# Optimization experiments

Measured on AMD Instinct MI355X. Metric: run time of the kernel, lower is better.

Reference implementation:

```python
import jax, jax.numpy as jnp
import numpy as np

NEG_SLOPE = 0.2

def _gat_conv(x, src, dst, W, a_src, a_dst, b, heads, out_ch, concat):
    N = x.shape[0]
    h = (x @ W).reshape(N, heads, out_ch)                      # [N,H,C]
    al_s = jnp.einsum('nhc,hc->nh', h, a_src)                  # [N,H]
    al_d = jnp.einsum('nhc,hc->nh', h, a_dst)
    e = jax.nn.leaky_relu(al_s[src] + al_d[dst], NEG_SLOPE)    # [E,H]
    emax = jax.ops.segment_max(e, dst, num_segments=N)         # [N,H]
    ex = jnp.exp(e - emax[dst])
    denom = jax.ops.segment_sum(ex, dst, num_segments=N)
    alpha = ex / denom[dst]                                    # [E,H]
    msg = h[src] * alpha[:, :, None]                           # [E,H,C]
    out = jax.ops.segment_sum(msg, dst, num_segments=N)        # [N,H,C]
    if concat:
        out = out.reshape(N, heads * out_ch)
    else:
        out = out.mean(axis=1)
    return out + b

def _add_self_loops(edge_index, N):
    loops = jnp.arange(N, dtype=edge_index.dtype)
    src = jnp.concatenate([edge_index[0], loops])
    dst = jnp.concatenate([edge_index[1], loops])
    return src, dst

def setup_inputs() -> dict:
    key = jax.random.key(0)
    ks = jax.random.split(key, 16)
    N, E, Fin, C, H, G, OUT = 50000, 1600000, 128, 32, 8, 256, 64
    s = 0.05
    inp = {
        'x': jax.random.normal(ks[0], (N, Fin), jnp.float32),
        'edge_index': jax.random.randint(ks[1], (2, E), 0, N, jnp.int64),
        'batch': jnp.sort(jax.random.randint(ks[2], (N,), 0, G, jnp.int64)),
        'W0': jax.random.normal(ks[3], (Fin, H * C), jnp.float32) * s,
        'a_src0': jax.random.normal(ks[4], (H, C), jnp.float32) * s,
        'a_dst0': jax.random.normal(ks[5], (H, C), jnp.float32) * s,
        'b0': jnp.zeros((H * C,), jnp.float32),
        'W1': jax.random.normal(ks[6], (H * C, H * C), jnp.float32) * s,
        'a_src1': jax.random.normal(ks[7], (H, C), jnp.float32) * s,
        'a_dst1': jax.random.normal(ks[8], (H, C), jnp.float32) * s,
        'b1': jnp.zeros((H * C,), jnp.float32),
        'W2': jax.random.normal(ks[9], (H * C, C), jnp.float32) * s,
        'a_src2': jax.random.normal(ks[10], (1, C), jnp.float32) * s,
        'a_dst2': jax.random.normal(ks[11], (1, C), jnp.float32) * s,
        'b2': jnp.zeros((C,), jnp.float32),
        'lin_w': jax.random.normal(ks[12], (C, OUT), jnp.float32) * s,
        'lin_b': jnp.zeros((OUT,), jnp.float32),
    }
    return inp

def reference(x, edge_index, batch, W0, a_src0, a_dst0, b0, W1, a_src1, a_dst1, b1,
              W2, a_src2, a_dst2, b2, lin_w, lin_b):
    N = x.shape[0]
    G = 256
    src, dst = _add_self_loops(edge_index, N)
    h = jax.nn.relu(_gat_conv(x, src, dst, W0, a_src0, a_dst0, b0, 8, 32, True))
    h = jax.nn.relu(_gat_conv(h, src, dst, W1, a_src1, a_dst1, b1, 8, 32, True))
    h = _gat_conv(h, src, dst, W2, a_src2, a_dst2, b2, 1, 32, True)  # heads=1 concat -> [N,32]
    # global mean pool over graphs
    sums = jax.ops.segment_sum(h, batch, num_segments=G)
    cnts = jax.ops.segment_sum(jnp.ones((N,), h.dtype), batch, num_segments=G)
    pooled = sums / jnp.maximum(cnts, 1.0)[:, None]
    return pooled @ lin_w + lin_b
```

## Files before the change

### kernel.cpp

```cpp
#include <hip/hip_runtime.h>
#include <hip/hip_bf16.h>


#define LRELU(x) ((x) >= 0.f ? (x) : 0.2f * (x))

typedef unsigned short ushort8 __attribute__((ext_vector_type(8)));
typedef unsigned short ushort4v __attribute__((ext_vector_type(4)));
typedef __attribute__((ext_vector_type(8))) short bf16x8;
typedef __attribute__((ext_vector_type(4))) float f32x4;

__device__ __forceinline__ float bf2f(unsigned short u) {
    return __uint_as_float(((unsigned)u) << 16);
}
__device__ __forceinline__ unsigned short f2bf(float f) {
    __hip_bfloat16 b = __float2bfloat16(f);
    return *reinterpret_cast<unsigned short*>(&b);
}
__device__ __forceinline__ void gl_lds16(const unsigned short* g, unsigned short* l) {
    __builtin_amdgcn_global_load_lds((const __attribute__((address_space(1))) void*)g,
                                     (__attribute__((address_space(3))) void*)l, 16, 0, 0);
}

#define NBUCK 16


__global__ void hist16_kernel(const int* __restrict__ src, const int* __restrict__ dst,
                              int* __restrict__ bcnt, int E, int N) {
    int i = blockIdx.x * blockDim.x + threadIdx.x;
    int s, d;
    if (i < E) { s = src[i]; d = dst[i]; }
    else if (i < E + N) { s = i - E; d = s; }
    else return;
    int b = (s * NBUCK) / N;
    atomicAdd(&bcnt[d * NBUCK + b], 1);
}

__global__ void node_deg_kernel(const int* __restrict__ bcnt, int* __restrict__ deg, int N) {
    int n = blockIdx.x * blockDim.x + threadIdx.x;
    if (n >= N) return;
    int s = 0;
#pragma unroll
    for (int b = 0; b < NBUCK; b++) s += bcnt[n * NBUCK + b];
    deg[n] = s;
}

__global__ void scan_kernel(const int* __restrict__ deg, int* __restrict__ rowptr,
                            int n) {
    __shared__ int partial[1024];
    const int tid = threadIdx.x;
    const int chunk = (n + 1023) / 1024;
    const int start = min(tid * chunk, n);
    const int end = min(start + chunk, n);
    int s = 0;
    for (int i = start; i < end; i++) s += deg[i];
    partial[tid] = s;
    __syncthreads();
    for (int o = 1; o < 1024; o <<= 1) {
        int v = (tid >= o) ? partial[tid - o] : 0;
        __syncthreads();
        partial[tid] += v;
        __syncthreads();
    }
    int run = (tid == 0) ? 0 : partial[tid - 1];
    for (int i = start; i < end; i++) { rowptr[i] = run; run += deg[i]; }
    if (tid == 0) rowptr[n] = partial[1023];
}

__global__ void bstart_fill_kernel(const int* __restrict__ bcnt, const int* __restrict__ rowptr,
                                   int* __restrict__ bstart, int N) {
    int n = blockIdx.x * blockDim.x + threadIdx.x;
    if (n >= N) return;
    int base = rowptr[n];
#pragma unroll
    for (int b = 0; b < NBUCK; b++) {
        bstart[n * NBUCK + b] = base;
        base += bcnt[n * NBUCK + b];
    }
}

__global__ void scatter_col_binned(const int* __restrict__ src, const int* __restrict__ dst,
                                   int* __restrict__ bstart, int* __restrict__ col,
                                   int E, int N, int lo, int hi) {
    int i = blockIdx.x * blockDim.x + threadIdx.x;
    int s, d;
    if (i < E) {
        d = dst[i];
        if (d < lo || d >= hi) return;
        s = src[i];
    } else if (i < E + N) {
        d = i - E;
        if (d < lo || d >= hi) return;
        s = d;
    } else return;
    int b = (s * NBUCK) / N;
    int pos = atomicAdd(&bstart[d * NBUCK + b], 1);
    col[pos] = s;
}

__global__ void expand_dst_kernel(const int* __restrict__ rowptr, int* __restrict__ dstA,
                                  int N) {
    int n = blockIdx.x * blockDim.x + threadIdx.x;
    if (n >= N) return;
    int r0 = rowptr[n];
    int r1 = rowptr[n + 1];
    for (int p = r0; p < r1; p++) dstA[p] = n;
}

__global__ void gstart_kernel(const int* __restrict__ batch, int* __restrict__ gstart,
                              int N, int G) {
    int g = blockIdx.x * blockDim.x + threadIdx.x;
    if (g > G) return;
    int lo = 0, hi = N;
    while (lo < hi) { int mid = (lo + hi) >> 1; if (batch[mid] < g) lo = mid + 1; else hi = mid; }
    gstart[g] = lo;
}


__global__ void split_plain_kernel(const float* __restrict__ X, unsigned short* __restrict__ h,
                                   unsigned short* __restrict__ l, int n) {
    int i = blockIdx.x * blockDim.x + threadIdx.x;
    if (i >= n) return;
    float v = X[i];
    unsigned short hb = f2bf(v);
    h[i] = hb;
    l[i] = f2bf(v - bf2f(hb));
}

__global__ void splitT_kernel(const float* __restrict__ W, unsigned short* __restrict__ th,
                              unsigned short* __restrict__ tl, int K, int N) {
    int i = blockIdx.x * blockDim.x + threadIdx.x;
    if (i >= N * K) return;
    int n = i / K, k = i - n * K;
    float v = W[(size_t)k * N + n];
    unsigned short hb = f2bf(v);
    th[i] = hb;
    tl[i] = f2bf(v - bf2f(hb));
}


template <int BM, int BN, int WM, int WN>
__global__ __launch_bounds__(256)
void gemm_mfma_v2(const unsigned short* __restrict__ Ah, const unsigned short* __restrict__ Al,
                  const unsigned short* __restrict__ Bth, const unsigned short* __restrict__ Btl,
                  unsigned short* __restrict__ Cc, int M, int N, int K) {
    constexpr int BK = 32;
    constexpr int MT = WM / 16, NT = WN / 16;
    constexpr int NWX = BN / WN;
    __shared__ __attribute__((aligned(16))) unsigned short Ha[BM][BK];
    __shared__ __attribute__((aligned(16))) unsigned short La[BM][BK];
    __shared__ __attribute__((aligned(16))) unsigned short Hb[BN][BK];
    __shared__ __attribute__((aligned(16))) unsigned short Lb[BN][BK];
    const int tid = threadIdx.x;
    const int lane = tid & 63;
    const int wave = tid >> 6;
    const int wx = wave % NWX, wy = wave / NWX;
    const int by = blockIdx.y * BM;
    const int bx = blockIdx.x * BN;
    const int r16 = lane & 15, kg = lane >> 4;
    const int srow = lane >> 2, sslot = lane & 3;

    f32x4 acc[MT][NT];
#pragma unroll
    for (int i = 0; i < MT; i++)
#pragma unroll
        for (int j = 0; j < NT; j++) acc[i][j] = (f32x4){0.f, 0.f, 0.f, 0.f};

    for (int k0 = 0; k0 < K; k0 += BK) {
        for (int t = wave; t < BM / 16; t += 4) {
            int gm = by + t * 16 + srow;
            if (gm >= M) gm = M - 1;
            const size_t goff = (size_t)gm * K + k0 + sslot * 8;
            gl_lds16(Ah + goff, &Ha[t * 16][0]);
            gl_lds16(Al + goff, &La[t * 16][0]);
        }
        for (int t = wave; t < BN / 16; t += 4) {
            int gn = bx + t * 16 + srow;
            const size_t goff = (size_t)gn * K + k0 + sslot * 8;
            gl_lds16(Bth + goff, &Hb[t * 16][0]);
            gl_lds16(Btl + goff, &Lb[t * 16][0]);
        }
        __syncthreads();
        bf16x8 bh[NT], bl[NT];
#pragma unroll
        for (int j = 0; j < NT; j++) {
            bh[j] = *(const bf16x8*)&Hb[wx * WN + j * 16 + r16][kg * 8];
            bl[j] = *(const bf16x8*)&Lb[wx * WN + j * 16 + r16][kg * 8];
        }
#pragma unroll
        for (int i = 0; i < MT; i++) {
            bf16x8 ah = *(const bf16x8*)&Ha[wy * WM + i * 16 + r16][kg * 8];
            bf16x8 al2 = *(const bf16x8*)&La[wy * WM + i * 16 + r16][kg * 8];
#pragma unroll
            for (int j = 0; j < NT; j++) {
                acc[i][j] = __builtin_amdgcn_mfma_f32_16x16x32_bf16(ah, bh[j], acc[i][j], 0, 0, 0);
                acc[i][j] = __builtin_amdgcn_mfma_f32_16x16x32_bf16(ah, bl[j], acc[i][j], 0, 0, 0);
                acc[i][j] = __builtin_amdgcn_mfma_f32_16x16x32_bf16(al2, bh[j], acc[i][j], 0, 0, 0);
            }
        }
        __syncthreads();
    }
#pragma unroll
    for (int i = 0; i < MT; i++) {
#pragma unroll
        for (int r = 0; r < 4; r++) {
            int gm = by + wy * WM + i * 16 + kg * 4 + r;
            if (gm >= M) continue;
#pragma unroll
            for (int j = 0; j < NT; j++) {
                int gn = bx + wx * WN + j * 16 + r16;
                Cc[(size_t)gm * N + gn] = f2bf(acc[i][j][r]);
            }
        }
    }
}


template <int H, int C>
__global__ void al_bf16(const unsigned short* __restrict__ hfeat, const float* __restrict__ a_src,
                        const float* __restrict__ a_dst, float* __restrict__ als,
                        float* __restrict__ ald, int N) {
    int i = blockIdx.x * blockDim.x + threadIdx.x;
    if (i >= N * H) return;
    int n = i / H, h = i % H;
    const unsigned short* hp = hfeat + (size_t)n * H * C + h * C;
    float s1 = 0.f, s2 = 0.f;
    for (int c0 = 0; c0 < C; c0 += 8) {
        ushort8 v = *(const ushort8*)(hp + c0);
#pragma unroll
        for (int k = 0; k < 8; k++) {
            float f = bf2f(v[k]);
            s1 += f * a_src[h * C + c0 + k];
            s2 += f * a_dst[h * C + c0 + k];
        }
    }
    als[i] = s1;
    ald[i] = s2;
}


__global__ void edge_w_pair(const float* __restrict__ als, const float* __restrict__ ald,
                            const int* __restrict__ col, const int* __restrict__ dstA,
                            unsigned int* __restrict__ wts2, int Etot) {
    int i = blockIdx.x * blockDim.x + threadIdx.x;
    if (i >= Etot * 4) return;
    int pos = i >> 2, hp = i & 3;
    int s = col[pos], d = dstA[pos];
    float2 a = *(const float2*)&als[(size_t)s * 8 + hp * 2];
    float2 b = *(const float2*)&ald[(size_t)d * 8 + hp * 2];
    float e0 = a.x + b.x; e0 = LRELU(e0);
    float e1 = a.y + b.y; e1 = LRELU(e1);
    unsigned lo = f2bf(__expf(e0));
    unsigned hi = f2bf(__expf(e1));
    wts2[i] = lo | (hi << 16);
}

__global__ void edge_w_h1(const float* __restrict__ als, const float* __restrict__ ald,
                          const int* __restrict__ col, const int* __restrict__ dstA,
                          unsigned short* __restrict__ wts, int Etot) {
    int i = blockIdx.x * blockDim.x + threadIdx.x;
    if (i >= Etot) return;
    int s = col[i], d = dstA[i];
    float e = als[s] + ald[d];
    e = LRELU(e);
    wts[i] = f2bf(__expf(e));
}


__global__ __launch_bounds__(256)
void gat_agg_w8(const unsigned short* __restrict__ hfeat,
                const unsigned short* __restrict__ wts,
                const int* __restrict__ rowptr,
                const int* __restrict__ col,
                const float* __restrict__ bias,
                unsigned short* __restrict__ outH, unsigned short* __restrict__ outL,
                int N) {
    constexpr int CAP = 128;
    const int wid = threadIdx.x >> 6;
    const int lane = threadIdx.x & 63;
    const int n = blockIdx.x * 4 + wid;
    __shared__ float se_all[4][CAP * 8];
    __shared__ int scol_all[4][CAP];
    if (n >= N) return;
    float* se = se_all[wid];
    int* scol = scol_all[wid];

    const int r0 = rowptr[n];
    const int deg = rowptr[n + 1] - r0;
    const int dh8 = deg * 8;
    const size_t wbase = (size_t)r0 * 8;
    const int dcap = min(deg, CAP);

    for (int j = lane; j < dcap; j += 64) scol[j] = col[r0 + j];

    float p0 = 0.f, p1 = 0.f, p2 = 0.f, p3 = 0.f, p4 = 0.f, p5 = 0.f, p6 = 0.f, p7 = 0.f;
    for (int base = 0; base < dh8; base += 512) {
        int idx = base + lane * 8;
        if (idx < dh8) {
            ushort8 v = *(const ushort8*)&wts[wbase + idx];
            float f0 = bf2f(v[0]), f1 = bf2f(v[1]), f2 = bf2f(v[2]), f3 = bf2f(v[3]);
            float f4 = bf2f(v[4]), f5 = bf2f(v[5]), f6 = bf2f(v[6]), f7 = bf2f(v[7]);
            p0 += f0; p1 += f1; p2 += f2; p3 += f3;
            p4 += f4; p5 += f5; p6 += f6; p7 += f7;
            if (idx < CAP * 8) {
                *(float4*)&se[idx] = (float4){f0, f1, f2, f3};
                *(float4*)&se[idx + 4] = (float4){f4, f5, f6, f7};
            }
        }
    }
#pragma unroll
    for (int m = 1; m < 64; m <<= 1) {
        p0 += __shfl_xor(p0, m); p1 += __shfl_xor(p1, m);
        p2 += __shfl_xor(p2, m); p3 += __shfl_xor(p3, m);
        p4 += __shfl_xor(p4, m); p5 += __shfl_xor(p5, m);
        p6 += __shfl_xor(p6, m); p7 += __shfl_xor(p7, m);
    }
    const int q = lane >> 3;
    float S = (q == 0) ? p0 : (q == 1) ? p1 : (q == 2) ? p2 : (q == 3) ? p3
            : (q == 4) ? p4 : (q == 5) ? p5 : (q == 6) ? p6 : p7;
    const float sinv = 1.0f / S;

    const int cb = lane * 4;
    float a0 = 0.f, a1 = 0.f, a2 = 0.f, a3 = 0.f;
    int j = 0;
    for (; j + 3 < dcap; j += 4) {
        int s0 = __builtin_amdgcn_readfirstlane(scol[j]);
        int s1 = __builtin_amdgcn_readfirstlane(scol[j + 1]);
        int s2 = __builtin_amdgcn_readfirstlane(scol[j + 2]);
        int s3 = __builtin_amdgcn_readfirstlane(scol[j + 3]);
        ushort4v v0 = *(const ushort4v*)(hfeat + (size_t)s0 * 256 + cb);
        ushort4v v1 = *(const ushort4v*)(hfeat + (size_t)s1 * 256 + cb);
        ushort4v v2 = *(const ushort4v*)(hfeat + (size_t)s2 * 256 + cb);
        ushort4v v3 = *(const ushort4v*)(hfeat + (size_t)s3 * 256 + cb);
        float w0 = se[j * 8 + q];
        float w1 = se[j * 8 + 8 + q];
        float w2 = se[j * 8 + 16 + q];
        float w3 = se[j * 8 + 24 + q];
        a0 += bf2f(v0[0]) * w0; a1 += bf2f(v0[1]) * w0; a2 += bf2f(v0[2]) * w0; a3 += bf2f(v0[3]) * w0;
        a0 += bf2f(v1[0]) * w1; a1 += bf2f(v1[1]) * w1; a2 += bf2f(v1[2]) * w1; a3 += bf2f(v1[3]) * w1;
        a0 += bf2f(v2[0]) * w2; a1 += bf2f(v2[1]) * w2; a2 += bf2f(v2[2]) * w2; a3 += bf2f(v2[3]) * w2;
        a0 += bf2f(v3[0]) * w3; a1 += bf2f(v3[1]) * w3; a2 += bf2f(v3[2]) * w3; a3 += bf2f(v3[3]) * w3;
    }
    for (; j < dcap; j++) {
        int s0 = __builtin_amdgcn_readfirstlane(scol[j]);
        ushort4v v0 = *(const ushort4v*)(hfeat + (size_t)s0 * 256 + cb);
        float w0 = se[j * 8 + q];
        a0 += bf2f(v0[0]) * w0; a1 += bf2f(v0[1]) * w0; a2 += bf2f(v0[2]) * w0; a3 += bf2f(v0[3]) * w0;
    }
    for (; j < deg; j++) {
        int s0 = col[r0 + j];
        float w0 = bf2f(wts[wbase + (size_t)j * 8 + q]);
        ushort4v v0 = *(const ushort4v*)(hfeat + (size_t)s0 * 256 + cb);
        a0 += bf2f(v0[0]) * w0; a1 += bf2f(v0[1]) * w0; a2 += bf2f(v0[2]) * w0; a3 += bf2f(v0[3]) * w0;
    }

    float4 b4 = *(const float4*)&bias[cb];
    float o0 = fmaxf(a0 * sinv + b4.x, 0.f);
    float o1 = fmaxf(a1 * sinv + b4.y, 0.f);
    float o2 = fmaxf(a2 * sinv + b4.z, 0.f);
    float o3 = fmaxf(a3 * sinv + b4.w, 0.f);
    unsigned short h0 = f2bf(o0), h1 = f2bf(o1), h2 = f2bf(o2), h3 = f2bf(o3);
    const size_t ob = (size_t)n * 256 + cb;
    *(ushort4v*)&outH[ob] = (ushort4v){h0, h1, h2, h3};
    *(ushort4v*)&outL[ob] = (ushort4v){f2bf(o0 - bf2f(h0)), f2bf(o1 - bf2f(h1)),
                                       f2bf(o2 - bf2f(h2)), f2bf(o3 - bf2f(h3))};
}


__global__ __launch_bounds__(256)
void gat_agg_h1w(const unsigned short* __restrict__ hfeat,
                 const unsigned short* __restrict__ wts,
                 const int* __restrict__ rowptr, const int* __restrict__ col,
                 const float* __restrict__ bias, float* __restrict__ out, int N) {
    constexpr int CAP = 256;
    const int wid = threadIdx.x >> 6;
    const int lane = threadIdx.x & 63;
    const int n = blockIdx.x * 4 + wid;
    __shared__ float sw_all[4][CAP];
    __shared__ int scol_all[4][CAP];
    if (n >= N) return;
    float* sw = sw_all[wid];
    int* scol = scol_all[wid];

    const int r0 = rowptr[n];
    const int deg = rowptr[n + 1] - r0;
    const int dcap = min(deg, CAP);

    float lsum = 0.f;
    for (int idx = lane; idx < deg; idx += 64) {
        float v = bf2f(wts[r0 + idx]);
        if (idx < CAP) { sw[idx] = v; scol[idx] = col[r0 + idx]; }
        lsum += v;
    }
#pragma unroll
    for (int m = 1; m < 64; m <<= 1) lsum += __shfl_xor(lsum, m);
    const float sinv = 1.0f / lsum;

    const int slot = lane >> 3, ch = lane & 7;
    float a0 = 0.f, a1 = 0.f, a2 = 0.f, a3 = 0.f;
    for (int j = 0; j < dcap; j += 8) {
        int e = j + slot;
        int ec = min(e, dcap - 1);
        int s = scol[ec];
        float w = (e < dcap) ? sw[ec] : 0.f;
        ushort4v v = *(const ushort4v*)(hfeat + (size_t)s * 32 + ch * 4);
        a0 += bf2f(v[0]) * w; a1 += bf2f(v[1]) * w;
        a2 += bf2f(v[2]) * w; a3 += bf2f(v[3]) * w;
    }
    for (int j = CAP; j < deg; j += 8) {
        int e = j + slot;
        int ec = min(e, deg - 1);
        int s = col[r0 + ec];
        float w = (e < deg) ? bf2f(wts[r0 + ec]) : 0.f;
        ushort4v v = *(const ushort4v*)(hfeat + (size_t)s * 32 + ch * 4);
        a0 += bf2f(v[0]) * w; a1 += bf2f(v[1]) * w;
        a2 += bf2f(v[2]) * w; a3 += bf2f(v[3]) * w;
    }
#pragma unroll
    for (int m = 8; m < 64; m <<= 1) {
        a0 += __shfl_xor(a0, m);
        a1 += __shfl_xor(a1, m);
        a2 += __shfl_xor(a2, m);
        a3 += __shfl_xor(a3, m);
    }
    if (slot == 0) {
        float4 b4 = *(const float4*)&bias[ch * 4];
        float4 o;
        o.x = a0 * sinv + b4.x;
        o.y = a1 * sinv + b4.y;
        o.z = a2 * sinv + b4.z;
        o.w = a3 * sinv + b4.w;
        *(float4*)&out[(size_t)n * 32 + ch * 4] = o;
    }
}


__global__ __launch_bounds__(256)
void pool_final_kernel(const float* __restrict__ h, const int* __restrict__ gstart,
                       const float* __restrict__ lin_w, const float* __restrict__ lin_b,
                       float* __restrict__ out) {
    const int g = blockIdx.x;
    const int tid = threadIdx.x;
    const int n0 = gstart[g], n1 = gstart[g + 1];
    const int r = tid >> 5, c = tid & 31;
    __shared__ float pp[4][32];
    __shared__ float pm[32];
    float acc = 0.f;
    for (int n = n0 + r; n < n1; n += 8) acc += h[(size_t)n * 32 + c];
    acc += __shfl_xor(acc, 32);
    if ((tid & 63) < 32) pp[tid >> 6][c] = acc;
    __syncthreads();
    if (tid < 32) {
        float s = pp[0][tid] + pp[1][tid] + pp[2][tid] + pp[3][tid];
        pm[tid] = s / fmaxf((float)(n1 - n0), 1.f);
    }
    __syncthreads();
    if (tid < 64) {
        float a = lin_b[tid];
#pragma unroll 8
        for (int cc = 0; cc < 32; cc++) a += pm[cc] * lin_w[cc * 64 + tid];
        out[(size_t)g * 64 + tid] = a;
    }
}


extern "C" void kernel_launch(void* const* d_in, const int* in_sizes, int n_in,
                              void* d_out, int out_size, void* d_ws, size_t ws_size,
                              hipStream_t stream) {
    const float* x     = (const float*)d_in[0];
    const int*   ei    = (const int*)d_in[1];
    const int*   batch = (const int*)d_in[2];
    const float* W0    = (const float*)d_in[3];
    const float* a_s0  = (const float*)d_in[4];
    const float* a_d0  = (const float*)d_in[5];
    const float* b0    = (const float*)d_in[6];
    const float* W1    = (const float*)d_in[7];
    const float* a_s1  = (const float*)d_in[8];
    const float* a_d1  = (const float*)d_in[9];
    const float* b1    = (const float*)d_in[10];
    const float* W2    = (const float*)d_in[11];
    const float* a_s2  = (const float*)d_in[12];
    const float* a_d2  = (const float*)d_in[13];
    const float* b2    = (const float*)d_in[14];
    const float* lin_w = (const float*)d_in[15];
    const float* lin_b = (const float*)d_in[16];

    const int N = in_sizes[0] / 128;
    const int E = in_sizes[1] / 2;
    const int G = 256;
    const int Etot = E + N;
    const int* src = ei;
    const int* dst = ei + E;

    char* w = (char*)d_ws;
    size_t off = 0;
    auto alloc = [&](size_t bytes) -> void* {
        void* p = (void*)(w + off);
        off += (bytes + 255) & ~(size_t)255;
        return p;
    };
    int* bcnt   = (int*)alloc((size_t)N * NBUCK * 4);
    int* bstart = (int*)alloc((size_t)N * NBUCK * 4);
    int* deg    = (int*)alloc((size_t)N * 4);
    int* rowptr = (int*)alloc((size_t)(N + 1) * 4);
    int* colA   = (int*)alloc((size_t)Etot * 4);
    int* dstA   = (int*)alloc((size_t)Etot * 4);
    int* gstart = (int*)alloc((size_t)(G + 1) * 4);
    float* als  = (float*)alloc((size_t)N * 8 * 4);
    float* ald  = (float*)alloc((size_t)N * 8 * 4);
    unsigned short* hb  = (unsigned short*)alloc((size_t)N * 256 * 2);
    unsigned short* wts = (unsigned short*)alloc((size_t)Etot * 8 * 2);
    unsigned short* g0h = (unsigned short*)alloc((size_t)N * 256 * 2);
    unsigned short* g0l = (unsigned short*)alloc((size_t)N * 256 * 2);
    float* out2 = (float*)alloc((size_t)N * 32 * 4);
    unsigned short* w0h = (unsigned short*)alloc((size_t)128 * 256 * 2);
    unsigned short* w0l = (unsigned short*)alloc((size_t)128 * 256 * 2);
    unsigned short* w1h = (unsigned short*)alloc((size_t)256 * 256 * 2);
    unsigned short* w1l = (unsigned short*)alloc((size_t)256 * 256 * 2);
    unsigned short* w2h = (unsigned short*)alloc((size_t)256 * 32 * 2);
    unsigned short* w2l = (unsigned short*)alloc((size_t)256 * 32 * 2);
    unsigned short* xh = g0h;
    unsigned short* xl = g0h + (size_t)N * 128;

    hipMemsetAsync(bcnt, 0, (size_t)N * NBUCK * 4, stream);

    hist16_kernel<<<(Etot + 255) / 256, 256, 0, stream>>>(src, dst, bcnt, E, N);
    node_deg_kernel<<<(N + 255) / 256, 256, 0, stream>>>(bcnt, deg, N);
    scan_kernel<<<1, 1024, 0, stream>>>(deg, rowptr, N);
    bstart_fill_kernel<<<(N + 255) / 256, 256, 0, stream>>>(bcnt, rowptr, bstart, N);
    for (int p = 0; p < 2; p++) {
        int lo = (int)((size_t)N * p / 2);
        int hi = (int)((size_t)N * (p + 1) / 2);
        scatter_col_binned<<<(Etot + 255) / 256, 256, 0, stream>>>(src, dst, bstart, colA, E, N, lo, hi);
    }
    expand_dst_kernel<<<(N + 255) / 256, 256, 0, stream>>>(rowptr, dstA, N);
    gstart_kernel<<<2, 256, 0, stream>>>(batch, gstart, N, G);

    split_plain_kernel<<<(N * 128 + 255) / 256, 256, 0, stream>>>(x, xh, xl, N * 128);
    splitT_kernel<<<(128 * 256 + 255) / 256, 256, 0, stream>>>(W0, w0h, w0l, 128, 256);
    splitT_kernel<<<(256 * 256 + 255) / 256, 256, 0, stream>>>(W1, w1h, w1l, 256, 256);
    splitT_kernel<<<(256 * 32 + 255) / 256, 256, 0, stream>>>(W2, w2h, w2l, 256, 32);

    const int MB = (N + 127) / 128;

    gemm_mfma_v2<128, 128, 64, 64><<<dim3(2, MB), 256, 0, stream>>>(xh, xl, w0h, w0l, hb, N, 256, 128);
    al_bf16<8, 32><<<(N * 8 + 255) / 256, 256, 0, stream>>>(hb, a_s0, a_d0, als, ald, N);
    edge_w_pair<<<((size_t)Etot * 4 + 255) / 256, 256, 0, stream>>>(als, ald, colA, dstA, (unsigned int*)wts, Etot);
    gat_agg_w8<<<(N + 3) / 4, 256, 0, stream>>>(hb, wts, rowptr, colA, b0, g0h, g0l, N);

    gemm_mfma_v2<128, 128, 64, 64><<<dim3(2, MB), 256, 0, stream>>>(g0h, g0l, w1h, w1l, hb, N, 256, 256);
    al_bf16<8, 32><<<(N * 8 + 255) / 256, 256, 0, stream>>>(hb, a_s1, a_d1, als, ald, N);
    edge_w_pair<<<((size_t)Etot * 4 + 255) / 256, 256, 0, stream>>>(als, ald, colA, dstA, (unsigned int*)wts, Etot);
    gat_agg_w8<<<(N + 3) / 4, 256, 0, stream>>>(hb, wts, rowptr, colA, b1, g0h, g0l, N);

    gemm_mfma_v2<128, 32, 32, 32><<<dim3(1, MB), 256, 0, stream>>>(g0h, g0l, w2h, w2l, hb, N, 32, 256);
    al_bf16<1, 32><<<(N + 255) / 256, 256, 0, stream>>>(hb, a_s2, a_d2, als, ald, N);
    edge_w_h1<<<(Etot + 255) / 256, 256, 0, stream>>>(als, ald, colA, dstA, wts, Etot);
    gat_agg_h1w<<<(N + 3) / 4, 256, 0, stream>>>(hb, wts, rowptr, colA, b2, out2, N);

    pool_final_kernel<<<G, 256, 0, stream>>>(out2, gstart, lin_w, lin_b, (float*)d_out);
}
```

Measured before the change: 693.7 us.

## Fuse edge-weight computation into aggregation and simplify CSR build

Drops the separate edge-weight kernels and the per-edge weight buffer. Each aggregation kernel now computes exp(leaky_relu(als[src]+ald[dst])) directly from the per-node attention scalars, which removes a full write and reread of Etot*8 bf16 weights per layer. The CSR construction also drops the 16-bucket source binning and the dstA expansion, using plain degree atomics and rowptr atomics as cursors. The risk is that loss of source-sorted column order within rows may hurt gather locality, and exp is recomputed in the tail loops beyond the cache capacity.

```diff
diff --git a/kernel.cpp b/kernel.cpp
--- a/kernel.cpp
+++ b/kernel.cpp
@@ -21,27 +21,12 @@
                                      (__attribute__((address_space(3))) void*)l, 16, 0, 0);
 }
 
-#define NBUCK 16
-
-
-__global__ void hist16_kernel(const int* __restrict__ src, const int* __restrict__ dst,
-                              int* __restrict__ bcnt, int E, int N) {
+
+__global__ void deg_kernel(const int* __restrict__ dst, int* __restrict__ deg,
+                           int E, int N) {
     int i = blockIdx.x * blockDim.x + threadIdx.x;
-    int s, d;
-    if (i < E) { s = src[i]; d = dst[i]; }
-    else if (i < E + N) { s = i - E; d = s; }
-    else return;
-    int b = (s * NBUCK) / N;
-    atomicAdd(&bcnt[d * NBUCK + b], 1);
-}
-
-__global__ void node_deg_kernel(const int* __restrict__ bcnt, int* __restrict__ deg, int N) {
-    int n = blockIdx.x * blockDim.x + threadIdx.x;
-    if (n >= N) return;
-    int s = 0;
-#pragma unroll
-    for (int b = 0; b < NBUCK; b++) s += bcnt[n * NBUCK + b];
-    deg[n] = s;
+    if (i < E) atomicAdd(&deg[dst[i]], 1);
+    else if (i < E + N) atomicAdd(&deg[i - E], 1);
 }
 
 __global__ void scan_kernel(const int* __restrict__ deg, int* __restrict__ rowptr,
@@ -66,44 +51,21 @@
     if (tid == 0) rowptr[n] = partial[1023];
 }
 
-__global__ void bstart_fill_kernel(const int* __restrict__ bcnt, const int* __restrict__ rowptr,
-                                   int* __restrict__ bstart, int N) {
-    int n = blockIdx.x * blockDim.x + threadIdx.x;
-    if (n >= N) return;
-    int base = rowptr[n];
-#pragma unroll
-    for (int b = 0; b < NBUCK; b++) {
-        bstart[n * NBUCK + b] = base;
-        base += bcnt[n * NBUCK + b];
-    }
-}
-
 __global__ void scatter_col_binned(const int* __restrict__ src, const int* __restrict__ dst,
-                                   int* __restrict__ bstart, int* __restrict__ col,
+                                   int* __restrict__ rowptr, int* __restrict__ col,
                                    int E, int N, int lo, int hi) {
     int i = blockIdx.x * blockDim.x + threadIdx.x;
-    int s, d;
     if (i < E) {
-        d = dst[i];
+        int d = dst[i];
         if (d < lo || d >= hi) return;
-        s = src[i];
+        int pos = atomicAdd(&rowptr[d], 1);
+        col[pos] = src[i];
     } else if (i < E + N) {
-        d = i - E;
+        int d = i - E;
         if (d < lo || d >= hi) return;
-        s = d;
-    } else return;
-    int b = (s * NBUCK) / N;
-    int pos = atomicAdd(&bstart[d * NBUCK + b], 1);
-    col[pos] = s;
-}
-
-__global__ void expand_dst_kernel(const int* __restrict__ rowptr, int* __restrict__ dstA,
-                                  int N) {
-    int n = blockIdx.x * blockDim.x + threadIdx.x;
-    if (n >= N) return;
-    int r0 = rowptr[n];
-    int r1 = rowptr[n + 1];
-    for (int p = r0; p < r1; p++) dstA[p] = n;
+        int pos = atomicAdd(&rowptr[d], 1);
+        col[pos] = d;
+    }
 }
 
 __global__ void gstart_kernel(const int* __restrict__ batch, int* __restrict__ gstart,
@@ -238,37 +200,9 @@
 }
 
 
-__global__ void edge_w_pair(const float* __restrict__ als, const float* __restrict__ ald,
-                            const int* __restrict__ col, const int* __restrict__ dstA,
-                            unsigned int* __restrict__ wts2, int Etot) {
-    int i = blockIdx.x * blockDim.x + threadIdx.x;
-    if (i >= Etot * 4) return;
-    int pos = i >> 2, hp = i & 3;
-    int s = col[pos], d = dstA[pos];
-    float2 a = *(const float2*)&als[(size_t)s * 8 + hp * 2];
-    float2 b = *(const float2*)&ald[(size_t)d * 8 + hp * 2];
-    float e0 = a.x + b.x; e0 = LRELU(e0);
-    float e1 = a.y + b.y; e1 = LRELU(e1);
-    unsigned lo = f2bf(__expf(e0));
-    unsigned hi = f2bf(__expf(e1));
-    wts2[i] = lo | (hi << 16);
-}
-
-__global__ void edge_w_h1(const float* __restrict__ als, const float* __restrict__ ald,
-                          const int* __restrict__ col, const int* __restrict__ dstA,
-                          unsigned short* __restrict__ wts, int Etot) {
-    int i = blockIdx.x * blockDim.x + threadIdx.x;
-    if (i >= Etot) return;
-    int s = col[i], d = dstA[i];
-    float e = als[s] + ald[d];
-    e = LRELU(e);
-    wts[i] = f2bf(__expf(e));
-}
-
-
 __global__ __launch_bounds__(256)
 void gat_agg_w8(const unsigned short* __restrict__ hfeat,
-                const unsigned short* __restrict__ wts,
+                const float* __restrict__ als, const float* __restrict__ ald,
                 const int* __restrict__ rowptr,
                 const int* __restrict__ col,
                 const float* __restrict__ bias,
@@ -284,40 +218,31 @@
     float* se = se_all[wid];
     int* scol = scol_all[wid];
 
-    const int r0 = rowptr[n];
-    const int deg = rowptr[n + 1] - r0;
-    const int dh8 = deg * 8;
-    const size_t wbase = (size_t)r0 * 8;
+    const int r0 = (n == 0) ? 0 : rowptr[n - 1];
+    const int deg = rowptr[n] - r0;
     const int dcap = min(deg, CAP);
 
     for (int j = lane; j < dcap; j += 64) scol[j] = col[r0 + j];
 
-    float p0 = 0.f, p1 = 0.f, p2 = 0.f, p3 = 0.f, p4 = 0.f, p5 = 0.f, p6 = 0.f, p7 = 0.f;
-    for (int base = 0; base < dh8; base += 512) {
-        int idx = base + lane * 8;
-        if (idx < dh8) {
-            ushort8 v = *(const ushort8*)&wts[wbase + idx];
-            float f0 = bf2f(v[0]), f1 = bf2f(v[1]), f2 = bf2f(v[2]), f3 = bf2f(v[3]);
-            float f4 = bf2f(v[4]), f5 = bf2f(v[5]), f6 = bf2f(v[6]), f7 = bf2f(v[7]);
-            p0 += f0; p1 += f1; p2 += f2; p3 += f3;
-            p4 += f4; p5 += f5; p6 += f6; p7 += f7;
-            if (idx < CAP * 8) {
-                *(float4*)&se[idx] = (float4){f0, f1, f2, f3};
-                *(float4*)&se[idx + 4] = (float4){f4, f5, f6, f7};
-            }
-        }
-    }
-#pragma unroll
-    for (int m = 1; m < 64; m <<= 1) {
-        p0 += __shfl_xor(p0, m); p1 += __shfl_xor(p1, m);
-        p2 += __shfl_xor(p2, m); p3 += __shfl_xor(p3, m);
-        p4 += __shfl_xor(p4, m); p5 += __shfl_xor(p5, m);
-        p6 += __shfl_xor(p6, m); p7 += __shfl_xor(p7, m);
-    }
+    const int slot = lane >> 3, h = lane & 7;
+    const float aldh = ald[(size_t)n * 8 + h];
+    float psum = 0.f;
+    for (int j = 0; j < deg; j += 8) {
+        int e = j + slot;
+        if (e < deg) {
+            int s = (e < dcap) ? scol[e] : col[r0 + e];
+            float ev = als[(size_t)s * 8 + h] + aldh;
+            ev = LRELU(ev);
+            float w = __expf(ev);
+            psum += w;
+            if (e < CAP) se[e * 8 + h] = w;
+        }
+    }
+#pragma unroll
+    for (int m = 8; m < 64; m <<= 1) psum += __shfl_xor(psum, m);
     const int q = lane >> 3;
-    float S = (q == 0) ? p0 : (q == 1) ? p1 : (q == 2) ? p2 : (q == 3) ? p3
-            : (q == 4) ? p4 : (q == 5) ? p5 : (q == 6) ? p6 : p7;
-    const float sinv = 1.0f / S;
+    const float sinv = 1.0f / __shfl(psum, q);
+    const float aldq = ald[(size_t)n * 8 + q];
 
     const int cb = lane * 4;
     float a0 = 0.f, a1 = 0.f, a2 = 0.f, a3 = 0.f;
@@ -348,7 +273,9 @@
     }
     for (; j < deg; j++) {
         int s0 = col[r0 + j];
-        float w0 = bf2f(wts[wbase + (size_t)j * 8 + q]);
+        float ev = als[(size_t)s0 * 8 + q] + aldq;
+        ev = LRELU(ev);
+        float w0 = __expf(ev);
         ushort4v v0 = *(const ushort4v*)(hfeat + (size_t)s0 * 256 + cb);
         a0 += bf2f(v0[0]) * w0; a1 += bf2f(v0[1]) * w0; a2 += bf2f(v0[2]) * w0; a3 += bf2f(v0[3]) * w0;
     }
@@ -368,7 +295,7 @@
 
 __global__ __launch_bounds__(256)
 void gat_agg_h1w(const unsigned short* __restrict__ hfeat,
-                 const unsigned short* __restrict__ wts,
+                 const float* __restrict__ als, const float* __restrict__ ald,
                  const int* __restrict__ rowptr, const int* __restrict__ col,
                  const float* __restrict__ bias, float* __restrict__ out, int N) {
     constexpr int CAP = 256;
@@ -381,15 +308,19 @@
     float* sw = sw_all[wid];
     int* scol = scol_all[wid];
 
-    const int r0 = rowptr[n];
-    const int deg = rowptr[n + 1] - r0;
+    const int r0 = (n == 0) ? 0 : rowptr[n - 1];
+    const int deg = rowptr[n] - r0;
     const int dcap = min(deg, CAP);
+    const float aldn = ald[n];
 
     float lsum = 0.f;
     for (int idx = lane; idx < deg; idx += 64) {
-        float v = bf2f(wts[r0 + idx]);
-        if (idx < CAP) { sw[idx] = v; scol[idx] = col[r0 + idx]; }
-        lsum += v;
+        int s = col[r0 + idx];
+        float ev = als[s] + aldn;
+        ev = LRELU(ev);
+        float w = __expf(ev);
+        if (idx < CAP) { sw[idx] = w; scol[idx] = s; }
+        lsum += w;
     }
 #pragma unroll
     for (int m = 1; m < 64; m <<= 1) lsum += __shfl_xor(lsum, m);
@@ -410,7 +341,12 @@
         int e = j + slot;
         int ec = min(e, deg - 1);
         int s = col[r0 + ec];
-        float w = (e < deg) ? bf2f(wts[r0 + ec]) : 0.f;
+        float w = 0.f;
+        if (e < deg) {
+            float ev = als[s] + aldn;
+            ev = LRELU(ev);
+            w = __expf(ev);
+        }
         ushort4v v = *(const ushort4v*)(hfeat + (size_t)s * 32 + ch * 4);
         a0 += bf2f(v[0]) * w; a1 += bf2f(v[1]) * w;
         a2 += bf2f(v[2]) * w; a3 += bf2f(v[3]) * w;
@@ -498,17 +434,13 @@
         off += (bytes + 255) & ~(size_t)255;
         return p;
     };
-    int* bcnt   = (int*)alloc((size_t)N * NBUCK * 4);
-    int* bstart = (int*)alloc((size_t)N * NBUCK * 4);
     int* deg    = (int*)alloc((size_t)N * 4);
     int* rowptr = (int*)alloc((size_t)(N + 1) * 4);
     int* colA   = (int*)alloc((size_t)Etot * 4);
-    int* dstA   = (int*)alloc((size_t)Etot * 4);
     int* gstart = (int*)alloc((size_t)(G + 1) * 4);
     float* als  = (float*)alloc((size_t)N * 8 * 4);
     float* ald  = (float*)alloc((size_t)N * 8 * 4);
     unsigned short* hb  = (unsigned short*)alloc((size_t)N * 256 * 2);
-    unsigned short* wts = (unsigned short*)alloc((size_t)Etot * 8 * 2);
     unsigned short* g0h = (unsigned short*)alloc((size_t)N * 256 * 2);
     unsigned short* g0l = (unsigned short*)alloc((size_t)N * 256 * 2);
     float* out2 = (float*)alloc((size_t)N * 32 * 4);
@@ -521,18 +453,15 @@
     unsigned short* xh = g0h;
     unsigned short* xl = g0h + (size_t)N * 128;
 
-    hipMemsetAsync(bcnt, 0, (size_t)N * NBUCK * 4, stream);
-
-    hist16_kernel<<<(Etot + 255) / 256, 256, 0, stream>>>(src, dst, bcnt, E, N);
-    node_deg_kernel<<<(N + 255) / 256, 256, 0, stream>>>(bcnt, deg, N);
+    hipMemsetAsync(deg, 0, (size_t)N * 4, stream);
+
+    deg_kernel<<<(Etot + 255) / 256, 256, 0, stream>>>(dst, deg, E, N);
     scan_kernel<<<1, 1024, 0, stream>>>(deg, rowptr, N);
-    bstart_fill_kernel<<<(N + 255) / 256, 256, 0, stream>>>(bcnt, rowptr, bstart, N);
     for (int p = 0; p < 2; p++) {
         int lo = (int)((size_t)N * p / 2);
         int hi = (int)((size_t)N * (p + 1) / 2);
-        scatter_col_binned<<<(Etot + 255) / 256, 256, 0, stream>>>(src, dst, bstart, colA, E, N, lo, hi);
-    }
-    expand_dst_kernel<<<(N + 255) / 256, 256, 0, stream>>>(rowptr, dstA, N);
+        scatter_col_binned<<<(Etot + 255) / 256, 256, 0, stream>>>(src, dst, rowptr, colA, E, N, lo, hi);
+    }
     gstart_kernel<<<2, 256, 0, stream>>>(batch, gstart, N, G);
 
     split_plain_kernel<<<(N * 128 + 255) / 256, 256, 0, stream>>>(x, xh, xl, N * 128);
@@ -544,18 +473,15 @@
 
     gemm_mfma_v2<128, 128, 64, 64><<<dim3(2, MB), 256, 0, stream>>>(xh, xl, w0h, w0l, hb, N, 256, 128);
     al_bf16<8, 32><<<(N * 8 + 255) / 256, 256, 0, stream>>>(hb, a_s0, a_d0, als, ald, N);
-    edge_w_pair<<<((size_t)Etot * 4 + 255) / 256, 256, 0, stream>>>(als, ald, colA, dstA, (unsigned int*)wts, Etot);
-    gat_agg_w8<<<(N + 3) / 4, 256, 0, stream>>>(hb, wts, rowptr, colA, b0, g0h, g0l, N);
+    gat_agg_w8<<<(N + 3) / 4, 256, 0, stream>>>(hb, als, ald, rowptr, colA, b0, g0h, g0l, N);
 
     gemm_mfma_v2<128, 128, 64, 64><<<dim3(2, MB), 256, 0, stream>>>(g0h, g0l, w1h, w1l, hb, N, 256, 256);
     al_bf16<8, 32><<<(N * 8 + 255) / 256, 256, 0, stream>>>(hb, a_s1, a_d1, als, ald, N);
-    edge_w_pair<<<((size_t)Etot * 4 + 255) / 256, 256, 0, stream>>>(als, ald, colA, dstA, (unsigned int*)wts, Etot);
-    gat_agg_w8<<<(N + 3) / 4, 256, 0, stream>>>(hb, wts, rowptr, colA, b1, g0h, g0l, N);
+    gat_agg_w8<<<(N + 3) / 4, 256, 0, stream>>>(hb, als, ald, rowptr, colA, b1, g0h, g0l, N);
 
     gemm_mfma_v2<128, 32, 32, 32><<<dim3(1, MB), 256, 0, stream>>>(g0h, g0l, w2h, w2l, hb, N, 32, 256);
     al_bf16<1, 32><<<(N + 255) / 256, 256, 0, stream>>>(hb, a_s2, a_d2, als, ald, N);
-    edge_w_h1<<<(Etot + 255) / 256, 256, 0, stream>>>(als, ald, colA, dstA, wts, Etot);
-    gat_agg_h1w<<<(N + 3) / 4, 256, 0, stream>>>(hb, wts, rowptr, colA, b2, out2, N);
+    gat_agg_h1w<<<(N + 3) / 4, 256, 0, stream>>>(hb, als, ald, rowptr, colA, b2, out2, N);
 
     pool_final_kernel<<<G, 256, 0, stream>>>(out2, gstart, lin_w, lin_b, (float*)d_out);
 }
```

After: 669.0 us. -3.6%, faster.
